# Performance work log

Hardware: AMD Instinct MI355X
Metric: run time of the kernel (lower is better)

Reference implementation:

```python
import jax, jax.numpy as jnp
import numpy as np

B, N = 8, 2048
D_MODEL, D_QK, NHEAD, N_K, D_FF = 256, 128, 8, 16, 1024
LN_EPS = 1e-5


def _layer_norm(x, g, b):
    m = jnp.mean(x, axis=-1, keepdims=True)
    v = jnp.var(x, axis=-1, keepdims=True)
    return (x - m) * jax.lax.rsqrt(v + LN_EPS) * g + b


def _l2_normalize(x):
    # F.normalize(dim=-1): x / max(||x||_2, 1e-12)
    n = jnp.sqrt(jnp.sum(x * x, axis=-1, keepdims=True))
    return x / jnp.maximum(n, 1e-12)


def setup_inputs() -> dict:
    key = jax.random.key(0)
    ks = jax.random.split(key, 12)
    s = 0.02
    return {
        "x": jax.random.normal(ks[0], (B, N, D_MODEL), dtype=jnp.float32),
        # linear_q / linear_k (d_model -> d_model_qk)
        "Wq": jax.random.normal(ks[1], (D_MODEL, D_QK), dtype=jnp.float32) * s,
        "bq": jnp.zeros((D_QK,), jnp.float32),
        "Wk": jax.random.normal(ks[2], (D_MODEL, D_QK), dtype=jnp.float32) * s,
        "bk": jnp.zeros((D_QK,), jnp.float32),
        # NoLinearQKMHA: value + output projections (d_model -> d_model)
        "Wv": jax.random.normal(ks[3], (D_MODEL, D_MODEL), dtype=jnp.float32) * s,
        "bv": jnp.zeros((D_MODEL,), jnp.float32),
        "Wo": jax.random.normal(ks[4], (D_MODEL, D_MODEL), dtype=jnp.float32) * s,
        "bo": jnp.zeros((D_MODEL,), jnp.float32),
        # norm1 (applied to gathered values)
        "g1": jnp.ones((D_MODEL,), jnp.float32),
        "b1": jnp.zeros((D_MODEL,), jnp.float32),
        # ffn: LayerNorm -> Linear -> GELU -> Linear
        "gf": jnp.ones((D_MODEL,), jnp.float32),
        "bf": jnp.zeros((D_MODEL,), jnp.float32),
        "W1": jax.random.normal(ks[5], (D_MODEL, D_FF), dtype=jnp.float32) * s,
        "b1f": jnp.zeros((D_FF,), jnp.float32),
        "W2": jax.random.normal(ks[6], (D_FF, D_MODEL), dtype=jnp.float32) * s,
        "b2f": jnp.zeros((D_MODEL,), jnp.float32),
        # residual_weight (init 0 in torch; nonzero here for a meaningful baseline)
        "rw": jnp.full((1,), 0.5, jnp.float32),
    }


def reference(x, Wq, bq, Wk, bk, Wv, bv, Wo, bo, g1, b1, gf, bf, W1, b1f, W2, b2f, rw):
    # --- project + normalize queries/keys ---
    qn = _l2_normalize(x @ Wq + bq)   # [B,N,Dqk]
    kn = _l2_normalize(x @ Wk + bk)   # [B,N,Dqk]

    # --- KNN: k smallest Euclidean distances from each query to keys ---
    d2 = (jnp.sum(qn * qn, -1)[:, :, None]
          + jnp.sum(kn * kn, -1)[:, None, :]
          - 2.0 * jnp.einsum('bqd,bkd->bqk', qn, kn))   # [B,N,N]
    _, idx = jax.lax.top_k(-d2, N_K)                     # [B,N,n_k]

    # --- gather neighbors ---
    gather = jax.vmap(lambda arr, ind: arr[ind])
    x_v = gather(x, idx)    # [B,N,n_k,D_MODEL]
    x_k = gather(kn, idx)   # [B,N,n_k,Dqk]

    # --- windowed MHA (NoLinearQK: q,k used directly; v projected) ---
    xnorm = _layer_norm(x_v, g1, b1)
    v = xnorm @ Wv + bv                                  # [B,N,n_k,D_MODEL]
    dh, dv = D_QK // NHEAD, D_MODEL // NHEAD
    qh = qn.reshape(B, N, NHEAD, dh)
    kh = x_k.reshape(B, N, N_K, NHEAD, dh)
    vh = v.reshape(B, N, N_K, NHEAD, dv)
    logits = jnp.einsum('bnhd,bnkhd->bnhk', qh, kh) / np.float32(np.sqrt(dh))
    attn = jax.nn.softmax(logits, axis=-1)
    o = jnp.einsum('bnhk,bnkhe->bnhe', attn, vh).reshape(B, N, D_MODEL)
    o = o @ Wo + bo

    # --- residuals (eval: dropout = identity) ---
    x = x + o * rw
    h = _layer_norm(x, gf, bf) @ W1 + b1f
    h = jax.nn.gelu(h, approximate=False) @ W2 + b2f
    x = x + h * rw
    return x
```

## Files before the change

### kernel.cpp

```cpp
#include <hip/hip_runtime.h>
#include <math.h>

#define BATCH 8
#define SEQ   2048
#define DM    256
#define DQK   128
#define NHEADS 8
#define NK    16
#define DFF   1024

typedef __attribute__((ext_vector_type(8))) short short8;
typedef __attribute__((ext_vector_type(8))) _Float16 half8;
typedef __attribute__((ext_vector_type(4))) float floatx4;
typedef unsigned long long ull;

__device__ __forceinline__ unsigned short f2bf(float f) {
    unsigned int u = __float_as_uint(f);
    u += 0x7fffu + ((u >> 16) & 1u);
    return (unsigned short)(u >> 16);
}

__device__ __forceinline__ float gelu_fast(float h) {
    float y = 0.7978845608028654f * (h + 0.044715f * h * h * h);
    float e = __expf(2.f * y);
    float t = 1.f - 2.f / (e + 1.f);
    return 0.5f * h * (1.f + t);
}

__device__ __forceinline__ ull mkkey(float f, int gidx) {
    unsigned int u = __float_as_uint(f);
    u ^= (unsigned int)((int)u >> 31) | 0x80000000u;
    return ((ull)u << 32) | (unsigned int)(2047 - gidx);
}

__device__ __forceinline__ ull shfl_xor_u64(ull v, int m) {
    unsigned int lo = (unsigned int)v, hi = (unsigned int)(v >> 32);
    lo = __shfl_xor(lo, m);
    hi = __shfl_xor(hi, m);
    return ((ull)hi << 32) | lo;
}

__global__ __launch_bounds__(256) void conv_kernel(
    const float* __restrict__ W1, const float* __restrict__ W2,
    const float* __restrict__ Wv, const float* __restrict__ Wo,
    unsigned short* __restrict__ W1f, unsigned short* __restrict__ W2f,
    unsigned short* __restrict__ Wvf, unsigned short* __restrict__ Wof)
{
    int g = blockIdx.x * 256 + threadIdx.x;
    const float* W; unsigned short* O; int e, stride;
    if (g < 32768)      { W = W1; O = W1f; e = g;         stride = DFF; }
    else if (g < 65536) { W = W2; O = W2f; e = g - 32768; stride = DM;  }
    else if (g < 73728) { W = Wv; O = Wvf; e = g - 65536; stride = DM;  }
    else                { W = Wo; O = Wof; e = g - 73728; stride = DM;  }
    int lane = e & 63;
    int kk, nt;
    if (g < 32768)      { kk = (e >> 6) & 7;  nt = e >> 9;  }
    else if (g < 65536) { kk = (e >> 6) & 31; nt = e >> 11; }
    else                { kk = (e >> 6) & 7;  nt = e >> 9;  }
    int n = nt * 16 + (lane & 15);
    int k0 = kk * 32 + (lane >> 4) * 8;
    unsigned int pk[4];
    #pragma unroll
    for (int jj = 0; jj < 4; ++jj) {
        unsigned short lo = f2bf(W[(size_t)(k0 + 2 * jj) * stride + n]);
        unsigned short hi = f2bf(W[(size_t)(k0 + 2 * jj + 1) * stride + n]);
        pk[jj] = (unsigned int)lo | ((unsigned int)hi << 16);
    }
    *(uint4*)(O + (size_t)e * 8) = make_uint4(pk[0], pk[1], pk[2], pk[3]);
}

__global__ __launch_bounds__(256) void proj_qk_kernel(
    const float* __restrict__ x,
    const float* __restrict__ Wq, const float* __restrict__ bq,
    const float* __restrict__ Wk, const float* __restrict__ bk,
    float* __restrict__ qn, float* __restrict__ kn,
    unsigned short* __restrict__ knTh, unsigned short* __restrict__ knTl,
    float* __restrict__ knsq)
{
    __shared__ __align__(16) float ks[8 * 128];
    __shared__ float nred[8][2], kred[8][2], k2red[8][2];

    const int tid = threadIdx.x;
    const int b = blockIdx.x & 7;
    const int chunk = blockIdx.x >> 3;
    const size_t t0 = (size_t)b * SEQ + (size_t)chunk * 8;

    {
        const int col = tid & 127, half = tid >> 7;
        const int half_u = __builtin_amdgcn_readfirstlane(half);
        const float* xrow[4];
        #pragma unroll
        for (int t = 0; t < 4; ++t)
            xrow[t] = x + (t0 + (size_t)(half_u * 4 + t)) * DM;

        float qa[4] = {0.f, 0.f, 0.f, 0.f}, ka[4] = {0.f, 0.f, 0.f, 0.f};
        for (int d = 0; d < 256; d += 4) {
            float4 xv[4];
            #pragma unroll
            for (int t = 0; t < 4; ++t) xv[t] = *(const float4*)(xrow[t] + d);
            #pragma unroll
            for (int dd = 0; dd < 4; ++dd) {
                float wq = Wq[(d + dd) * DQK + col];
                float wk = Wk[(d + dd) * DQK + col];
                #pragma unroll
                for (int t = 0; t < 4; ++t) {
                    float xval = (dd == 0) ? xv[t].x : (dd == 1) ? xv[t].y
                               : (dd == 2) ? xv[t].z : xv[t].w;
                    qa[t] = fmaf(xval, wq, qa[t]);
                    ka[t] = fmaf(xval, wk, ka[t]);
                }
            }
        }
        #pragma unroll
        for (int t = 0; t < 4; ++t) { qa[t] += bq[col]; ka[t] += bk[col]; }

        const int sub = (tid >> 6) & 1;
        #pragma unroll
        for (int t = 0; t < 4; ++t) {
            float sq = qa[t] * qa[t], sk = ka[t] * ka[t];
            #pragma unroll
            for (int m = 1; m < 64; m <<= 1) { sq += __shfl_xor(sq, m); sk += __shfl_xor(sk, m); }
            if ((tid & 63) == 0) { nred[half * 4 + t][sub] = sq; kred[half * 4 + t][sub] = sk; }
        }
        __syncthreads();
        float kvv[4];
        #pragma unroll
        for (int t = 0; t < 4; ++t) {
            int tok = half * 4 + t;
            float nq = sqrtf(nred[tok][0] + nred[tok][1]);
            float nk = sqrtf(kred[tok][0] + kred[tok][1]);
            float qv = qa[t] / fmaxf(nq, 1e-12f);
            float kv = ka[t] / fmaxf(nk, 1e-12f);
            qn[(t0 + tok) * DQK + col] = qv;
            kn[(t0 + tok) * DQK + col] = kv;
            ks[tok * 128 + col] = kv;
            kvv[t] = kv;
        }
        #pragma unroll
        for (int t = 0; t < 4; ++t) {
            float s2 = kvv[t] * kvv[t];
            #pragma unroll
            for (int m = 1; m < 64; m <<= 1) s2 += __shfl_xor(s2, m);
            if ((tid & 63) == 0) k2red[half * 4 + t][sub] = s2;
        }
        __syncthreads();
        if (tid < 8) knsq[t0 + tid] = k2red[tid][0] + k2red[tid][1];
    }

    {
        const int e   = tid & 127;
        const int sel = tid >> 7;
        const int key = e & 7;
        const int kq  = e >> 3;
        const int kk  = kq >> 2, qd = kq & 3;
        const int nt  = chunk >> 1;
        const int n   = ((chunk & 1) << 3) + key;
        const float* src = &ks[key * 128 + kk * 32 + qd * 8];
        unsigned int pk[4];
        #pragma unroll
        for (int jj = 0; jj < 4; ++jj) {
            float v0 = src[2 * jj], v1 = src[2 * jj + 1];
            _Float16 h0 = (_Float16)v0, h1 = (_Float16)v1;
            unsigned short u0, u1;
            if (sel == 0) {
                u0 = __builtin_bit_cast(unsigned short, h0);
                u1 = __builtin_bit_cast(unsigned short, h1);
            } else {
                _Float16 l0 = (_Float16)((v0 - (float)h0) * 4096.f);
                _Float16 l1 = (_Float16)((v1 - (float)h1) * 4096.f);
                u0 = __builtin_bit_cast(unsigned short, l0);
                u1 = __builtin_bit_cast(unsigned short, l1);
            }
            pk[jj] = (unsigned int)u0 | ((unsigned int)u1 << 16);
        }
        unsigned short* dst = (sel ? knTl : knTh)
            + (size_t)b * 262144
            + (size_t)((nt * 4 + kk) * 64 + qd * 16 + n) * 8;
        *(uint4*)dst = make_uint4(pk[0], pk[1], pk[2], pk[3]);
    }
}

__global__ __launch_bounds__(256) void proj_v_kernel(
    const float* __restrict__ x,
    const float* __restrict__ bv, const float* __restrict__ g1,
    const float* __restrict__ b1,
    const unsigned short* __restrict__ Wvf, float* __restrict__ vall)
{
    __shared__ __align__(16) float xs[16][260];
    __shared__ float stat_m[16], stat_r[16];
    __shared__ float bvs[256], g1s[256], b1s[256];

    const int tid = threadIdx.x;
    const int lane = tid & 63, wave = tid >> 6;
    const int quad = lane >> 4, lr = lane & 15;
    const size_t t0 = (size_t)blockIdx.x * 16;

    for (int i = tid; i < 16 * 256; i += 256) xs[i >> 8][i & 255] = x[t0 * DM + i];
    bvs[tid] = bv[tid]; g1s[tid] = g1[tid]; b1s[tid] = b1[tid];
    __syncthreads();

    {
        int tok = tid >> 4, l = tid & 15;
        float s = 0.f, s2 = 0.f;
        #pragma unroll
        for (int i = 0; i < 16; ++i) {
            float v = xs[tok][l + 16 * i];
            s += v; s2 += v * v;
        }
        #pragma unroll
        for (int m = 1; m < 16; m <<= 1) { s += __shfl_xor(s, m); s2 += __shfl_xor(s2, m); }
        if (l == 0) {
            float mean = s * (1.f / 256.f);
            float var  = s2 * (1.f / 256.f) - mean * mean;
            stat_m[tok] = mean;
            stat_r[tok] = rsqrtf(var + 1e-5f);
        }
    }
    __syncthreads();

    short8 av[8];
    {
        float mm = stat_m[lr], rr = stat_r[lr];
        #pragma unroll
        for (int kk = 0; kk < 8; ++kk) {
            #pragma unroll
            for (int j = 0; j < 8; ++j) {
                int k = kk * 32 + quad * 8 + j;
                float v = (xs[lr][k] - mm) * rr * g1s[k] + b1s[k];
                av[kk][j] = (short)f2bf(v);
            }
        }
    }
    floatx4 acc[4];
    #pragma unroll
    for (int nt = 0; nt < 4; ++nt) acc[nt] = (floatx4){0.f, 0.f, 0.f, 0.f};
    #pragma unroll
    for (int nt = 0; nt < 4; ++nt) {
        #pragma unroll
        for (int kk = 0; kk < 8; ++kk) {
            short8 bfr = *(const short8*)(Wvf + ((size_t)(((wave * 4 + nt) * 8 + kk) * 64) + lane) * 8);
            acc[nt] = __builtin_amdgcn_mfma_f32_16x16x32_bf16(av[kk], bfr, acc[nt], 0, 0, 0);
        }
    }
    #pragma unroll
    for (int nt = 0; nt < 4; ++nt) {
        int col = (wave * 4 + nt) * 16 + lr;
        float bb = bvs[col];
        #pragma unroll
        for (int reg = 0; reg < 4; ++reg) {
            int row = quad * 4 + reg;
            vall[(t0 + row) * DM + col] = acc[nt][reg] + bb;
        }
    }
}

__global__ __launch_bounds__(256, 4) void attn_kernel(
    const float* __restrict__ x,
    const float* __restrict__ qn_g, const float* __restrict__ kn_g,
    const unsigned short* __restrict__ knTh, const unsigned short* __restrict__ knTl,
    const float* __restrict__ knsq_g,
    const float* __restrict__ vall,
    const unsigned short* __restrict__ Wof, const float* __restrict__ bo,
    const float* __restrict__ rw, float* __restrict__ out)
{
    __shared__ __align__(16) float s_ld[16 * 512];
    float* attn_s = s_ld;
    float* o8     = s_ld + 2048;

    const int tid = threadIdx.x;
    const int lane = tid & 63, wave = tid >> 6;
    const int quad = lane >> 4, lr = lane & 15;
    const int sg = lane >> 5, sl = lane & 31;
    const int sgid = wave * 2 + sg;
    const int b = blockIdx.x & 7;
    const int chunk = blockIdx.x >> 3;
    const size_t tq0 = (size_t)b * SEQ + (size_t)chunk * 16;
    const size_t rowb = (size_t)b * SEQ;

    half8 a_hi[4], a_lo[4];
    {
        const float* qrow = qn_g + (tq0 + lr) * DQK + quad * 8;
        #pragma unroll
        for (int kk = 0; kk < 4; ++kk) {
            float4 fa = *(const float4*)(qrow + kk * 32);
            float4 fb = *(const float4*)(qrow + kk * 32 + 4);
            float vv[8] = {fa.x, fa.y, fa.z, fa.w, fb.x, fb.y, fb.z, fb.w};
            #pragma unroll
            for (int j = 0; j < 8; ++j) {
                float v = vv[j];
                _Float16 h = (_Float16)v;
                a_hi[kk][j] = h;
                a_lo[kk][j] = (_Float16)((v - (float)h) * 4096.f);
            }
        }
    }

    const unsigned short* bh = knTh + (size_t)b * 262144;
    const unsigned short* bl = knTl + (size_t)b * 262144;
    const float* ksqb = knsq_g + rowb;

    ull c0[2], c1[2];

    for (int q4 = 0; q4 < 4; ++q4) {
        if (q4) __syncthreads();

        for (int t = 0; t < 8; ++t) {
            const int tile = q4 * 32 + wave * 8 + t;
            const unsigned short* ph = bh + (size_t)tile * 2048 + lane * 8;
            const unsigned short* pl = bl + (size_t)tile * 2048 + lane * 8;
            floatx4 am  = (floatx4){0.f, 0.f, 0.f, 0.f};
            floatx4 ax1 = (floatx4){0.f, 0.f, 0.f, 0.f};
            floatx4 ax2 = (floatx4){0.f, 0.f, 0.f, 0.f};
            #pragma unroll
            for (int kk = 0; kk < 4; ++kk) {
                half8 bhf = *(const half8*)(ph + kk * 512);
                half8 blf = *(const half8*)(pl + kk * 512);
                am  = __builtin_amdgcn_mfma_f32_16x16x32_f16(a_hi[kk], bhf, am,  0, 0, 0);
                ax1 = __builtin_amdgcn_mfma_f32_16x16x32_f16(a_hi[kk], blf, ax1, 0, 0, 0);
                ax2 = __builtin_amdgcn_mfma_f32_16x16x32_f16(a_lo[kk], bhf, ax2, 0, 0, 0);
            }
            const int keyloc = (wave * 8 + t) * 16 + lr;
            const float kq = ksqb[q4 * 512 + keyloc];
            #pragma unroll
            for (int r = 0; r < 4; ++r) {
                s_ld[(quad * 4 + r) * 512 + keyloc] =
                    2.f * (am[r] + (ax1[r] + ax2[r]) * (1.f / 4096.f)) - kq;
            }
        }
        __syncthreads();

        #pragma unroll
        for (int qi = 0; qi < 2; ++qi) {
            const int q = sgid + 8 * qi;
            const float* srow = &s_ld[q * 512 + sl];
            float f0 = -INFINITY, f1 = -INFINITY;
            int   i0 = 0, i1 = 0;
            #pragma unroll
            for (int i = 0; i < 16; ++i) {
                float f = srow[32 * i];
                int gidx = q4 * 512 + sl + 32 * i;
                bool a  = f > f0;
                bool bb = f > f1;
                f1 = a ? f0 : (bb ? f    : f1);
                i1 = a ? i0 : (bb ? gidx : i1);
                f0 = a ? f    : f0;
                i0 = a ? gidx : i0;
            }
            ull k2v = mkkey(f1, i1);
            ull cur = mkkey(f0, i0);
            int cnt = 0;
            for (int r = 0; r < NK; ++r) {
                ull w = cur;
                #pragma unroll
                for (int m = 1; m < 32; m <<= 1) {
                    ull o = shfl_xor_u64(w, m);
                    if (o > w) w = o;
                }
                const int slot = q4 * 16 + r;
                if (sl == slot)      c0[qi] = w;
                if (sl == slot - 32) c1[qi] = w;
                if (cur == w) {
                    ++cnt;
                    if (cnt == 1) cur = k2v;
                    else {
                        ull best = 0;
                        #pragma unroll
                        for (int i = 0; i < 16; ++i) {
                            float f = srow[32 * i];
                            ull k = mkkey(f, q4 * 512 + sl + 32 * i);
                            if (k < w && k > best) best = k;
                        }
                        cur = best;
                    }
                }
            }
        }
    }
    __syncthreads();

    int tidx[2] = {0, 0};
    #pragma unroll
    for (int qi = 0; qi < 2; ++qi) {
        ull ca = c0[qi], cb = c1[qi];
        ull hi = ca > cb ? ca : cb;
        ull lo = ca > cb ? cb : ca;
        ull cur = hi;
        int cnt = 0;
        for (int r = 0; r < NK; ++r) {
            ull w = cur;
            #pragma unroll
            for (int m = 1; m < 32; m <<= 1) {
                ull o = shfl_xor_u64(w, m);
                if (o > w) w = o;
            }
            if (sl == r) tidx[qi] = 2047 - (int)(unsigned int)(w & 0xFFFFFFFFull);
            if (cur == w) { ++cnt; cur = (cnt == 1) ? lo : 0ull; }
        }
    }

    #pragma unroll
    for (int qq = 0; qq < 4; ++qq) {
        const int sgq = qq & 1;
        const int qiq = qq >> 1;
        const int q   = wave * 2 + sgq + 8 * qiq;
        const int srcb = sgq * 32;
        const int h = lane >> 3;
        const int k1 = lane & 7, k2 = 8 + (lane & 7);
        const int i1 = __shfl(tidx[qiq], srcb + k1);
        const int i2 = __shfl(tidx[qiq], srcb + k2);
        const float* qrow = qn_g + (tq0 + q) * DQK + h * 16;
        const float* kr1 = kn_g + (rowb + i1) * DQK + h * 16;
        const float* kr2 = kn_g + (rowb + i2) * DQK + h * 16;
        float lg1 = 0.f, lg2 = 0.f;
        #pragma unroll
        for (int d = 0; d < 16; d += 4) {
            float4 qv = *(const float4*)&qrow[d];
            float4 a1 = *(const float4*)&kr1[d];
            float4 a2 = *(const float4*)&kr2[d];
            lg1 = fmaf(qv.x, a1.x, lg1); lg1 = fmaf(qv.y, a1.y, lg1);
            lg1 = fmaf(qv.z, a1.z, lg1); lg1 = fmaf(qv.w, a1.w, lg1);
            lg2 = fmaf(qv.x, a2.x, lg2); lg2 = fmaf(qv.y, a2.y, lg2);
            lg2 = fmaf(qv.z, a2.z, lg2); lg2 = fmaf(qv.w, a2.w, lg2);
        }
        lg1 *= 0.25f; lg2 *= 0.25f;
        float mx = fmaxf(lg1, lg2);
        #pragma unroll
        for (int m = 1; m < 8; m <<= 1) mx = fmaxf(mx, __shfl_xor(mx, m));
        float e1 = expf(lg1 - mx), e2 = expf(lg2 - mx);
        float ssum = e1 + e2;
        #pragma unroll
        for (int m = 1; m < 8; m <<= 1) ssum += __shfl_xor(ssum, m);
        attn_s[q * 128 + h * 16 + k1] = e1 / ssum;
        attn_s[q * 128 + h * 16 + k2] = e2 / ssum;

        float o[4] = {0.f, 0.f, 0.f, 0.f};
        for (int k = 0; k < NK; ++k) {
            const int ik = __shfl(tidx[qiq], srcb + k);
            const float* vr = vall + (rowb + ik) * DM;
            #pragma unroll
            for (int j = 0; j < 4; ++j) {
                int d = lane + 64 * j;
                o[j] = fmaf(attn_s[q * 128 + (d >> 5) * 16 + k], vr[d], o[j]);
            }
        }
        #pragma unroll
        for (int j = 0; j < 4; ++j) o8[q * 260 + lane + 64 * j] = o[j];
    }
    __syncthreads();

    {
        short8 ao[8];
        #pragma unroll
        for (int kk = 0; kk < 8; ++kk) {
            #pragma unroll
            for (int j = 0; j < 8; ++j) {
                int k = kk * 32 + quad * 8 + j;
                ao[kk][j] = (short)f2bf(o8[lr * 260 + k]);
            }
        }
        floatx4 aw[4];
        #pragma unroll
        for (int nt = 0; nt < 4; ++nt) aw[nt] = (floatx4){0.f, 0.f, 0.f, 0.f};
        #pragma unroll
        for (int nt = 0; nt < 4; ++nt) {
            #pragma unroll
            for (int kk = 0; kk < 8; ++kk) {
                short8 bofr = *(const short8*)(Wof + ((size_t)(((wave * 4 + nt) * 8 + kk) * 64) + lane) * 8);
                aw[nt] = __builtin_amdgcn_mfma_f32_16x16x32_bf16(ao[kk], bofr, aw[nt], 0, 0, 0);
            }
        }
        float rwv = rw[0];
        #pragma unroll
        for (int nt = 0; nt < 4; ++nt) {
            int col = (wave * 4 + nt) * 16 + lr;
            float bov = bo[col];
            #pragma unroll
            for (int reg = 0; reg < 4; ++reg) {
                int row = quad * 4 + reg;
                size_t t = tq0 + row;
                out[t * DM + col] = x[t * DM + col] + (aw[nt][reg] + bov) * rwv;
            }
        }
    }
}

__global__ __launch_bounds__(512, 4) void ffn_kernel(
    float* __restrict__ io,
    const float* __restrict__ gf, const float* __restrict__ bf,
    const unsigned short* __restrict__ W1f, const float* __restrict__ b1f,
    const unsigned short* __restrict__ W2f, const float* __restrict__ b2f,
    const float* __restrict__ rw)
{
    __shared__ __align__(16) char pool[66048];
    __shared__ float gfs[256], bfs[256], b2s[256], b1s[1024];
    __shared__ float stat_m[32], stat_r[32];

    float (*xs)[260] = (float(*)[260])pool;
    unsigned short (*Af)[8 * 64 * 8] = (unsigned short(*)[8 * 64 * 8])(pool + 33280);
    unsigned short (*G)[1032] = (unsigned short(*)[1032])pool;

    const int tid = threadIdx.x;
    const int lane = tid & 63, wave = tid >> 6;
    const int quad = lane >> 4, lr = lane & 15;
    const size_t t0 = (size_t)blockIdx.x * 32;

    for (int i = tid; i < 32 * 256; i += 512) xs[i >> 8][i & 255] = io[t0 * DM + i];
    if (tid < 256) { gfs[tid] = gf[tid]; bfs[tid] = bf[tid]; b2s[tid] = b2f[tid]; }
    for (int i = tid; i < 1024; i += 512) b1s[i] = b1f[i];
    __syncthreads();

    {
        int tok = tid >> 4, l = tid & 15;
        float s = 0.f, s2 = 0.f;
        #pragma unroll
        for (int i = 0; i < 16; ++i) {
            float v = xs[tok][l + 16 * i];
            s += v; s2 += v * v;
        }
        #pragma unroll
        for (int m = 1; m < 16; m <<= 1) { s += __shfl_xor(s, m); s2 += __shfl_xor(s2, m); }
        if (l == 0) {
            float mean = s * (1.f / 256.f);
            float var  = s2 * (1.f / 256.f) - mean * mean;
            stat_m[tok] = mean;
            stat_r[tok] = rsqrtf(var + 1e-5f);
        }
    }
    __syncthreads();

    {
        const int rt = wave >> 2;
        for (int kk = wave & 3; kk < 8; kk += 4) {
            int m = rt * 16 + lr, k0 = kk * 32 + quad * 8;
            float mm = stat_m[m], rr = stat_r[m];
            unsigned int pk[4];
            #pragma unroll
            for (int jj = 0; jj < 4; ++jj) {
                int ka = k0 + 2 * jj, kb = ka + 1;
                float v0 = (xs[m][ka] - mm) * rr * gfs[ka] + bfs[ka];
                float v1 = (xs[m][kb] - mm) * rr * gfs[kb] + bfs[kb];
                pk[jj] = (unsigned int)f2bf(v0) | ((unsigned int)f2bf(v1) << 16);
            }
            *(uint4*)&Af[rt][(kk * 64 + lane) * 8] = make_uint4(pk[0], pk[1], pk[2], pk[3]);
        }
    }
    __syncthreads();

    short8 afr[2][8];
    #pragma unroll
    for (int rt = 0; rt < 2; ++rt)
        #pragma unroll
        for (int kk = 0; kk < 8; ++kk)
            afr[rt][kk] = *(const short8*)&Af[rt][(kk * 64 + lane) * 8];
    __syncthreads();

    for (int nt = 0; nt < 8; ++nt) {
        floatx4 acc0 = (floatx4){0.f, 0.f, 0.f, 0.f};
        floatx4 acc1 = (floatx4){0.f, 0.f, 0.f, 0.f};
        const int ntg = wave * 8 + nt;
        #pragma unroll
        for (int kk = 0; kk < 8; ++kk) {
            short8 bfr = *(const short8*)(W1f + (size_t)((ntg * 8 + kk) * 64 + lane) * 8);
            acc0 = __builtin_amdgcn_mfma_f32_16x16x32_bf16(afr[0][kk], bfr, acc0, 0, 0, 0);
            acc1 = __builtin_amdgcn_mfma_f32_16x16x32_bf16(afr[1][kk], bfr, acc1, 0, 0, 0);
        }
        const int n = ntg * 16 + lr;
        const float bb = b1s[n];
        #pragma unroll
        for (int reg = 0; reg < 4; ++reg) {
            int row = quad * 4 + reg;
            G[row][n]      = f2bf(gelu_fast(acc0[reg] + bb));
            G[row + 16][n] = f2bf(gelu_fast(acc1[reg] + bb));
        }
    }
    __syncthreads();

    floatx4 acc2[2][2];
    #pragma unroll
    for (int nt2 = 0; nt2 < 2; ++nt2)
        #pragma unroll
        for (int rt = 0; rt < 2; ++rt)
            acc2[nt2][rt] = (floatx4){0.f, 0.f, 0.f, 0.f};

    for (int kk2 = 0; kk2 < 32; ++kk2) {
        short8 a20 = *(const short8*)&G[lr][kk2 * 32 + quad * 8];
        short8 a21 = *(const short8*)&G[16 + lr][kk2 * 32 + quad * 8];
        #pragma unroll
        for (int nt2 = 0; nt2 < 2; ++nt2) {
            short8 b2 = *(const short8*)(W2f + (size_t)((((wave * 2 + nt2) * 32 + kk2) * 64 + lane) * 8));
            acc2[nt2][0] = __builtin_amdgcn_mfma_f32_16x16x32_bf16(a20, b2, acc2[nt2][0], 0, 0, 0);
            acc2[nt2][1] = __builtin_amdgcn_mfma_f32_16x16x32_bf16(a21, b2, acc2[nt2][1], 0, 0, 0);
        }
    }

    float rwv = rw[0];
    #pragma unroll
    for (int nt2 = 0; nt2 < 2; ++nt2) {
        int col = (wave * 2 + nt2) * 16 + lr;
        float bb = b2s[col];
        #pragma unroll
        for (int rt = 0; rt < 2; ++rt) {
            #pragma unroll
            for (int reg = 0; reg < 4; ++reg) {
                int row = rt * 16 + quad * 4 + reg;
                float o = acc2[nt2][rt][reg] + bb;
                size_t idx = (t0 + row) * DM + col;
                io[idx] = io[idx] + o * rwv;
            }
        }
    }
}

extern "C" void kernel_launch(void* const* d_in, const int* in_sizes, int n_in,
                              void* d_out, int out_size, void* d_ws, size_t ws_size,
                              hipStream_t stream)
{
    const float* x   = (const float*)d_in[0];
    const float* Wq  = (const float*)d_in[1];
    const float* bq  = (const float*)d_in[2];
    const float* Wk  = (const float*)d_in[3];
    const float* bk  = (const float*)d_in[4];
    const float* Wv  = (const float*)d_in[5];
    const float* bv  = (const float*)d_in[6];
    const float* Wo  = (const float*)d_in[7];
    const float* bo  = (const float*)d_in[8];
    const float* g1  = (const float*)d_in[9];
    const float* b1  = (const float*)d_in[10];
    const float* gf  = (const float*)d_in[11];
    const float* bf  = (const float*)d_in[12];
    const float* W1  = (const float*)d_in[13];
    const float* b1f = (const float*)d_in[14];
    const float* W2  = (const float*)d_in[15];
    const float* b2f = (const float*)d_in[16];
    const float* rw  = (const float*)d_in[17];
    float* out = (float*)d_out;

    float* ws   = (float*)d_ws;
    float* qn   = ws;
    float* kn   = ws + 2097152;
    unsigned short* knTh = (unsigned short*)(ws + 4194304);
    unsigned short* knTl = knTh + 2097152;
    float* vall = ws + 6291456;
    float* knsq = ws + 10485760;
    unsigned short* W1f = (unsigned short*)(ws + 10502144);
    unsigned short* W2f = W1f + 262144;
    unsigned short* Wvf = W2f + 262144;
    unsigned short* Wof = Wvf + 65536;

    conv_kernel<<<320, 256, 0, stream>>>(W1, W2, Wv, Wo, W1f, W2f, Wvf, Wof);
    proj_qk_kernel<<<BATCH * SEQ / 8, 256, 0, stream>>>(x, Wq, bq, Wk, bk,
                                                        qn, kn, knTh, knTl, knsq);
    proj_v_kernel<<<BATCH * SEQ / 16, 256, 0, stream>>>(x, bv, g1, b1, Wvf, vall);
    attn_kernel<<<BATCH * SEQ / 16, 256, 0, stream>>>(x, qn, kn, knTh, knTl, knsq, vall,
                                                      Wof, bo, rw, out);
    ffn_kernel<<<BATCH * SEQ / 32, 512, 0, stream>>>(out, gf, bf, W1f, b1f, W2f, b2f, rw);
}
```

Before: 339.2 us.

## Fuse FFN into attention kernel to skip intermediate output round trip

The separate FFN kernel is merged into the attention kernel. Each 16-token block now runs layer norm, W1+GELU and W2 on its attention output in shared memory, keeps the residual in registers, and writes the final result once. This removes a kernel launch and the global write and re-read of the intermediate activations. In exchange, FFN tiles shrink from 32 to 16 rows, so each block re-streams W1/W2 for half as many tokens. The attention kernel also gains register and shared-memory pressure.

Measured after the change: 332.4 us. -2.0%, faster.

```diff
diff --git a/kernel.cpp b/kernel.cpp
--- a/kernel.cpp
+++ b/kernel.cpp
@@ -254,18 +254,26 @@
     }
 }
 
-__global__ __launch_bounds__(256, 4) void attn_kernel(
+__global__ __launch_bounds__(256, 4) void attn_ffn_kernel(
     const float* __restrict__ x,
     const float* __restrict__ qn_g, const float* __restrict__ kn_g,
     const unsigned short* __restrict__ knTh, const unsigned short* __restrict__ knTl,
     const float* __restrict__ knsq_g,
     const float* __restrict__ vall,
     const unsigned short* __restrict__ Wof, const float* __restrict__ bo,
+    const float* __restrict__ gf, const float* __restrict__ bf,
+    const unsigned short* __restrict__ W1f, const float* __restrict__ b1f,
+    const unsigned short* __restrict__ W2f, const float* __restrict__ b2f,
     const float* __restrict__ rw, float* __restrict__ out)
 {
-    __shared__ __align__(16) float s_ld[16 * 512];
+    __shared__ __align__(16) char pool[33024];
+    __shared__ float stat_m[16], stat_r[16];
+    float* s_ld   = (float*)pool;
     float* attn_s = s_ld;
     float* o8     = s_ld + 2048;
+    float (*xs2)[260] = (float(*)[260])pool;
+    unsigned short* Af = (unsigned short*)(pool + 16640);
+    unsigned short (*G)[1032] = (unsigned short(*)[1032])pool;
 
     const int tid = threadIdx.x;
     const int lane = tid & 63, wave = tid >> 6;
@@ -448,6 +456,8 @@
     }
     __syncthreads();
 
+    float rwv = rw[0];
+    float oval[4][4];
     {
         short8 ao[8];
         #pragma unroll
@@ -458,6 +468,7 @@
                 ao[kk][j] = (short)f2bf(o8[lr * 260 + k]);
             }
         }
+        __syncthreads();
         floatx4 aw[4];
         #pragma unroll
         for (int nt = 0; nt < 4; ++nt) aw[nt] = (floatx4){0.f, 0.f, 0.f, 0.f};
@@ -469,7 +480,6 @@
                 aw[nt] = __builtin_amdgcn_mfma_f32_16x16x32_bf16(ao[kk], bofr, aw[nt], 0, 0, 0);
             }
         }
-        float rwv = rw[0];
         #pragma unroll
         for (int nt = 0; nt < 4; ++nt) {
             int col = (wave * 4 + nt) * 16 + lr;
@@ -477,36 +487,12 @@
             #pragma unroll
             for (int reg = 0; reg < 4; ++reg) {
                 int row = quad * 4 + reg;
-                size_t t = tq0 + row;
-                out[t * DM + col] = x[t * DM + col] + (aw[nt][reg] + bov) * rwv;
-            }
-        }
-    }
-}
-
-__global__ __launch_bounds__(512, 4) void ffn_kernel(
-    float* __restrict__ io,
-    const float* __restrict__ gf, const float* __restrict__ bf,
-    const unsigned short* __restrict__ W1f, const float* __restrict__ b1f,
-    const unsigned short* __restrict__ W2f, const float* __restrict__ b2f,
-    const float* __restrict__ rw)
-{
-    __shared__ __align__(16) char pool[66048];
-    __shared__ float gfs[256], bfs[256], b2s[256], b1s[1024];
-    __shared__ float stat_m[32], stat_r[32];
-
-    float (*xs)[260] = (float(*)[260])pool;
-    unsigned short (*Af)[8 * 64 * 8] = (unsigned short(*)[8 * 64 * 8])(pool + 33280);
-    unsigned short (*G)[1032] = (unsigned short(*)[1032])pool;
-
-    const int tid = threadIdx.x;
-    const int lane = tid & 63, wave = tid >> 6;
-    const int quad = lane >> 4, lr = lane & 15;
-    const size_t t0 = (size_t)blockIdx.x * 32;
-
-    for (int i = tid; i < 32 * 256; i += 512) xs[i >> 8][i & 255] = io[t0 * DM + i];
-    if (tid < 256) { gfs[tid] = gf[tid]; bfs[tid] = bf[tid]; b2s[tid] = b2f[tid]; }
-    for (int i = tid; i < 1024; i += 512) b1s[i] = b1f[i];
+                float v = x[(tq0 + row) * DM + col] + (aw[nt][reg] + bov) * rwv;
+                oval[nt][reg] = v;
+                xs2[row][col] = v;
+            }
+        }
+    }
     __syncthreads();
 
     {
@@ -514,7 +500,7 @@
         float s = 0.f, s2 = 0.f;
         #pragma unroll
         for (int i = 0; i < 16; ++i) {
-            float v = xs[tok][l + 16 * i];
+            float v = xs2[tok][l + 16 * i];
             s += v; s2 += v * v;
         }
         #pragma unroll
@@ -528,85 +514,66 @@
     }
     __syncthreads();
 
-    {
-        const int rt = wave >> 2;
-        for (int kk = wave & 3; kk < 8; kk += 4) {
-            int m = rt * 16 + lr, k0 = kk * 32 + quad * 8;
-            float mm = stat_m[m], rr = stat_r[m];
-            unsigned int pk[4];
-            #pragma unroll
-            for (int jj = 0; jj < 4; ++jj) {
-                int ka = k0 + 2 * jj, kb = ka + 1;
-                float v0 = (xs[m][ka] - mm) * rr * gfs[ka] + bfs[ka];
-                float v1 = (xs[m][kb] - mm) * rr * gfs[kb] + bfs[kb];
-                pk[jj] = (unsigned int)f2bf(v0) | ((unsigned int)f2bf(v1) << 16);
-            }
-            *(uint4*)&Af[rt][(kk * 64 + lane) * 8] = make_uint4(pk[0], pk[1], pk[2], pk[3]);
-        }
-    }
-    __syncthreads();
-
-    short8 afr[2][8];
-    #pragma unroll
-    for (int rt = 0; rt < 2; ++rt)
-        #pragma unroll
-        for (int kk = 0; kk < 8; ++kk)
-            afr[rt][kk] = *(const short8*)&Af[rt][(kk * 64 + lane) * 8];
-    __syncthreads();
-
-    for (int nt = 0; nt < 8; ++nt) {
-        floatx4 acc0 = (floatx4){0.f, 0.f, 0.f, 0.f};
-        floatx4 acc1 = (floatx4){0.f, 0.f, 0.f, 0.f};
-        const int ntg = wave * 8 + nt;
+    for (int kk = wave; kk < 8; kk += 4) {
+        int m = lr, k0 = kk * 32 + quad * 8;
+        float mm = stat_m[m], rr = stat_r[m];
+        unsigned int pk[4];
+        #pragma unroll
+        for (int jj = 0; jj < 4; ++jj) {
+            int ka = k0 + 2 * jj, kb = ka + 1;
+            float v0 = (xs2[m][ka] - mm) * rr * gf[ka] + bf[ka];
+            float v1 = (xs2[m][kb] - mm) * rr * gf[kb] + bf[kb];
+            pk[jj] = (unsigned int)f2bf(v0) | ((unsigned int)f2bf(v1) << 16);
+        }
+        *(uint4*)&Af[(kk * 64 + lane) * 8] = make_uint4(pk[0], pk[1], pk[2], pk[3]);
+    }
+    __syncthreads();
+
+    short8 afr[8];
+    #pragma unroll
+    for (int kk = 0; kk < 8; ++kk)
+        afr[kk] = *(const short8*)&Af[(kk * 64 + lane) * 8];
+    __syncthreads();
+
+    for (int nt = 0; nt < 16; ++nt) {
+        floatx4 acc = (floatx4){0.f, 0.f, 0.f, 0.f};
+        const int ntg = wave * 16 + nt;
         #pragma unroll
         for (int kk = 0; kk < 8; ++kk) {
             short8 bfr = *(const short8*)(W1f + (size_t)((ntg * 8 + kk) * 64 + lane) * 8);
-            acc0 = __builtin_amdgcn_mfma_f32_16x16x32_bf16(afr[0][kk], bfr, acc0, 0, 0, 0);
-            acc1 = __builtin_amdgcn_mfma_f32_16x16x32_bf16(afr[1][kk], bfr, acc1, 0, 0, 0);
+            acc = __builtin_amdgcn_mfma_f32_16x16x32_bf16(afr[kk], bfr, acc, 0, 0, 0);
         }
         const int n = ntg * 16 + lr;
-        const float bb = b1s[n];
+        const float bb = b1f[n];
         #pragma unroll
         for (int reg = 0; reg < 4; ++reg) {
             int row = quad * 4 + reg;
-            G[row][n]      = f2bf(gelu_fast(acc0[reg] + bb));
-            G[row + 16][n] = f2bf(gelu_fast(acc1[reg] + bb));
-        }
-    }
-    __syncthreads();
-
-    floatx4 acc2[2][2];
-    #pragma unroll
-    for (int nt2 = 0; nt2 < 2; ++nt2)
-        #pragma unroll
-        for (int rt = 0; rt < 2; ++rt)
-            acc2[nt2][rt] = (floatx4){0.f, 0.f, 0.f, 0.f};
-
+            G[row][n] = f2bf(gelu_fast(acc[reg] + bb));
+        }
+    }
+    __syncthreads();
+
+    floatx4 acc2[4];
+    #pragma unroll
+    for (int nt2 = 0; nt2 < 4; ++nt2) acc2[nt2] = (floatx4){0.f, 0.f, 0.f, 0.f};
     for (int kk2 = 0; kk2 < 32; ++kk2) {
-        short8 a20 = *(const short8*)&G[lr][kk2 * 32 + quad * 8];
-        short8 a21 = *(const short8*)&G[16 + lr][kk2 * 32 + quad * 8];
-        #pragma unroll
-        for (int nt2 = 0; nt2 < 2; ++nt2) {
-            short8 b2 = *(const short8*)(W2f + (size_t)((((wave * 2 + nt2) * 32 + kk2) * 64 + lane) * 8));
-            acc2[nt2][0] = __builtin_amdgcn_mfma_f32_16x16x32_bf16(a20, b2, acc2[nt2][0], 0, 0, 0);
-            acc2[nt2][1] = __builtin_amdgcn_mfma_f32_16x16x32_bf16(a21, b2, acc2[nt2][1], 0, 0, 0);
-        }
-    }
-
-    float rwv = rw[0];
-    #pragma unroll
-    for (int nt2 = 0; nt2 < 2; ++nt2) {
-        int col = (wave * 2 + nt2) * 16 + lr;
-        float bb = b2s[col];
-        #pragma unroll
-        for (int rt = 0; rt < 2; ++rt) {
-            #pragma unroll
-            for (int reg = 0; reg < 4; ++reg) {
-                int row = rt * 16 + quad * 4 + reg;
-                float o = acc2[nt2][rt][reg] + bb;
-                size_t idx = (t0 + row) * DM + col;
-                io[idx] = io[idx] + o * rwv;
-            }
+        short8 a2 = *(const short8*)&G[lr][kk2 * 32 + quad * 8];
+        #pragma unroll
+        for (int nt2 = 0; nt2 < 4; ++nt2) {
+            short8 b2 = *(const short8*)(W2f + (size_t)((((wave * 4 + nt2) * 32 + kk2) * 64 + lane) * 8));
+            acc2[nt2] = __builtin_amdgcn_mfma_f32_16x16x32_bf16(a2, b2, acc2[nt2], 0, 0, 0);
+        }
+    }
+
+    #pragma unroll
+    for (int nt2 = 0; nt2 < 4; ++nt2) {
+        int col = (wave * 4 + nt2) * 16 + lr;
+        float bb = b2f[col];
+        #pragma unroll
+        for (int reg = 0; reg < 4; ++reg) {
+            int row = quad * 4 + reg;
+            float o = acc2[nt2][reg] + bb;
+            out[(tq0 + row) * DM + col] = oval[nt2][reg] + o * rwv;
         }
     }
 }
@@ -651,7 +618,7 @@
     proj_qk_kernel<<<BATCH * SEQ / 8, 256, 0, stream>>>(x, Wq, bq, Wk, bk,
                                                         qn, kn, knTh, knTl, knsq);
     proj_v_kernel<<<BATCH * SEQ / 16, 256, 0, stream>>>(x, bv, g1, b1, Wvf, vall);
-    attn_kernel<<<BATCH * SEQ / 16, 256, 0, stream>>>(x, qn, kn, knTh, knTl, knsq, vall,
-                                                      Wof, bo, rw, out);
-    ffn_kernel<<<BATCH * SEQ / 32, 512, 0, stream>>>(out, gf, bf, W1f, b1f, W2f, b2f, rw);
-}
+    attn_ffn_kernel<<<BATCH * SEQ / 16, 256, 0, stream>>>(
+        x, qn, kn, knTh, knTl, knsq, vall, Wof, bo,
+        gf, bf, W1f, b1f, W2f, b2f, rw, out);
+}
```
